# Optimization experiments

Hardware: AMD Instinct MI355X
Metric: run time of the kernel (lower is better)

The kernel has to match this reference:

```python
import jax, jax.numpy as jnp
import numpy as np

H, DK, DV, DEMB = 16, 64, 64, 1024
D_MODEL = H * DV


def setup_inputs() -> dict:
    key = jax.random.key(0)
    ks = jax.random.split(key, 9)
    scale = 0.02
    x = jax.random.normal(ks[0], (4, 2048, DEMB), dtype=jnp.float32)
    wq = jax.random.normal(ks[1], (DEMB, H * DK), dtype=jnp.float32) * scale
    bq = jnp.zeros((H * DK,), dtype=jnp.float32)
    wk = jax.random.normal(ks[2], (DEMB, H * DK), dtype=jnp.float32) * scale
    bk = jnp.zeros((H * DK,), dtype=jnp.float32)
    wv = jax.random.normal(ks[3], (DEMB, H * DV), dtype=jnp.float32) * scale
    bv = jnp.zeros((H * DV,), dtype=jnp.float32)
    wo = jax.random.normal(ks[4], (D_MODEL, D_MODEL), dtype=jnp.float32) * scale
    bo = jnp.zeros((D_MODEL,), dtype=jnp.float32)
    return {"x": x, "wq": wq, "bq": bq, "wk": wk, "bk": bk,
            "wv": wv, "bv": bv, "wo": wo, "bo": bo, "mask": 0}


def _split_heads(t, h):
    # (b, s, h*d) -> (b, h, s, d)
    b, s, _ = t.shape
    return t.reshape(b, s, h, -1).transpose(0, 2, 1, 3)


def reference(x, wq, bq, wk, bk, wv, bv, wo, bo, mask):
    b, s, _ = x.shape
    qs = _split_heads(x @ wq + bq, H)  # (b, h, s, dk)
    ks = _split_heads(x @ wk + bk, H)
    vs = _split_heads(x @ wv + bv, H)  # (b, h, s, dv)
    # FAITHFUL quirk: original scales by 1/sqrt(len(ks[0])) == 1/sqrt(n_heads),
    # not 1/sqrt(d_k).
    scores = jnp.einsum('bhqd,bhkd->bhqk', qs, ks) / jnp.sqrt(jnp.float32(H))
    # FAITHFUL quirk: masked_fill(mask == 0, ...) with scalar bool mask is a
    # no-op (True == 0 is False), so no masking is ever applied.
    attn = jax.nn.softmax(scores, axis=-1)
    out = jnp.einsum('bhqk,bhkd->bhqd', attn, vs)  # (b, h, s, dv)
    out = out.transpose(0, 2, 1, 3).reshape(b, s, D_MODEL)
    return out @ wo + bo
```

## Files before the change

### kernel.cpp

```cpp
#include <hip/hip_runtime.h>
#include <stdint.h>

typedef __attribute__((ext_vector_type(8))) short short8;
typedef __attribute__((ext_vector_type(4))) short short4v;
typedef __attribute__((ext_vector_type(4))) float floatx4;
typedef __attribute__((ext_vector_type(8))) _Float16 half8;
typedef __attribute__((ext_vector_type(2))) __fp16 pk2;

#define SEQ 2048
#define NTOK 8192
#define QSCALE 0.360673760222241f

__device__ __forceinline__ float b2f(unsigned short u){
  union { unsigned int i; float f; } v; v.i = ((unsigned int)u) << 16; return v.f;
}
__device__ __forceinline__ unsigned short f2b(float f){
  union { float f; unsigned int i; } v; v.f = f;
  unsigned int r = v.i + 0x7fffu + ((v.i >> 16) & 1u);
  return (unsigned short)(r >> 16);
}
__device__ __forceinline__ void async16(const unsigned short* g, unsigned short* l){
  __builtin_amdgcn_global_load_lds(
      (const __attribute__((address_space(1))) unsigned int*)g,
      (__attribute__((address_space(3))) unsigned int*)l, 16, 0, 0);
}

__global__ __launch_bounds__(256) void prep_kernel(
    const float* __restrict__ x,
    const float* __restrict__ wq, const float* __restrict__ wk,
    const float* __restrict__ wv, const float* __restrict__ wo,
    const float* __restrict__ bq, const float* __restrict__ bk,
    const float* __restrict__ bv,
    unsigned short* __restrict__ xb,
    unsigned short* __restrict__ wqkvT, unsigned short* __restrict__ woT,
    float* __restrict__ bqkv)
{
  __shared__ unsigned short lT[64][72];
  const int bid = blockIdx.x;
  const int tid = threadIdx.x;
  if (bid < 8192){
    int i = (bid*256 + tid)*4;
    float4 v = *(const float4*)(x + i);
    short4v o;
    o[0] = (short)f2b(v.x); o[1] = (short)f2b(v.y);
    o[2] = (short)f2b(v.z); o[3] = (short)f2b(v.w);
    *(short4v*)(xb + i) = o;
  } else if (bid < 9216){
    int idx = bid - 8192;
    int sel = idx >> 8, rest = idx & 255;
    const float* src = (sel==0)?wq:(sel==1)?wk:(sel==2)?wv:wo;
    unsigned short* dst = (sel<3) ? (wqkvT + (size_t)sel*1024*1024) : woT;
    int n0 = (rest & 15) * 64, k0 = (rest >> 4) * 64;
#pragma unroll
    for (int i=0;i<4;i++){
      int ch = tid + i*256;
      int r = ch>>4, c = (ch&15)*4;
      float4 v = *(const float4*)(src + (size_t)(k0+r)*1024 + n0 + c);
      lT[r][c+0] = f2b(v.x); lT[r][c+1] = f2b(v.y);
      lT[r][c+2] = f2b(v.z); lT[r][c+3] = f2b(v.w);
    }
    __syncthreads();
#pragma unroll
    for (int i=0;i<2;i++){
      int ch = tid + i*256;
      int rn = ch>>3, c = (ch&7)*8;
      short8 v;
#pragma unroll
      for (int j=0;j<8;j++) v[j] = (short)lT[c+j][rn];
      *(short8*)(dst + (size_t)(n0+rn)*1024 + k0 + c) = v;
    }
  } else {
    int i = (bid - 9216)*256 + tid;
    if (i < 3072){
      int sel = i >> 10, j = i & 1023;
      bqkv[i] = (sel==0)?bq[j]:(sel==1)?bk[j]:bv[j];
    }
  }
}

template<int MODE>
__global__ __launch_bounds__(256) void gemm_bt_kernel(
    const unsigned short* __restrict__ A,
    const unsigned short* __restrict__ Bt,
    const float* __restrict__ bias,
    void* __restrict__ Cv,
    unsigned short* __restrict__ Vt,
    int M, int N, int K)
{
  __shared__ unsigned short lA[128*64];
  __shared__ unsigned short lB[128*64];
  const int tid  = threadIdx.x;
  const int lane = tid & 63;
  const int wave = tid >> 6;
  const int quad = lane >> 4;
  const int l15  = lane & 15;
  const int wR = (wave >> 1) * 64;
  const int wC = (wave & 1) * 64;
  const int rowB = blockIdx.y * 128;
  const int colB = blockIdx.x * 128;

  const int srow = wave*32 + (lane>>3);
  const int sc8  = (lane&7) ^ (lane>>3);
  const unsigned short* gA = A  + (size_t)(rowB + srow)*K + sc8*8;
  const unsigned short* gB = Bt + (size_t)(colB + srow)*K + sc8*8;
  unsigned short* lAw = lA + wave*32*64 + lane*8;
  unsigned short* lBw = lB + wave*32*64 + lane*8;

  floatx4 acc[4][4];
#pragma unroll
  for (int t=0;t<4;t++)
#pragma unroll
    for (int u=0;u<4;u++) acc[t][u] = (floatx4){0.f,0.f,0.f,0.f};

  for (int kt = 0; kt < K; kt += 64){
    __syncthreads();
#pragma unroll
    for (int i=0;i<4;i++){
      async16(gA + (size_t)i*8*K + kt, lAw + i*512);
      async16(gB + (size_t)i*8*K + kt, lBw + i*512);
    }
    __syncthreads();
#pragma unroll
    for (int ks=0; ks<2; ks++){
      const int cph = ((ks*4 + quad) ^ (l15 & 7)) * 8;
      short8 af[4], bf[4];
#pragma unroll
      for (int t=0;t<4;t++) af[t] = *(const short8*)&lA[(wR + t*16 + l15)*64 + cph];
#pragma unroll
      for (int u=0;u<4;u++) bf[u] = *(const short8*)&lB[(wC + u*16 + l15)*64 + cph];
#pragma unroll
      for (int t=0;t<4;t++)
#pragma unroll
        for (int u=0;u<4;u++)
          acc[t][u] = __builtin_amdgcn_mfma_f32_16x16x32_bf16(af[t], bf[u], acc[t][u], 0, 0, 0);
    }
  }
  if (MODE == 3 && colB >= 2048){
#pragma unroll
    for (int u=0;u<4;u++){
      int col = colB + wC + u*16 + l15;
      float bval = bias[col];
      int vcol = col - 2048;
      int hh = vcol >> 6, dv = vcol & 63;
#pragma unroll
      for (int t=0;t<4;t++){
        int row0 = rowB + wR + t*16 + quad*4;
        int bb = row0 >> 11, s = row0 & 2047;
        union { pk2 p[2]; short4v s4; } cv;
        cv.p[0] = __builtin_amdgcn_cvt_pkrtz(acc[t][u][0]+bval, acc[t][u][1]+bval);
        cv.p[1] = __builtin_amdgcn_cvt_pkrtz(acc[t][u][2]+bval, acc[t][u][3]+bval);
        *(short4v*)(Vt + ((size_t)(bb*16+hh)*64 + dv)*2048 + s) = cv.s4;
      }
    }
  } else {
#pragma unroll
    for (int u=0;u<4;u++){
      int col = colB + wC + u*16 + l15;
      float bval = bias[col];
      float scale = (MODE == 3 && col < 1024) ? QSCALE : 1.0f;
#pragma unroll
      for (int t=0;t<4;t++){
        int row0 = rowB + wR + t*16 + quad*4;
#pragma unroll
        for (int r=0;r<4;r++){
          float val = (acc[t][u][r] + bval) * scale;
          if (MODE == 1) ((float*)Cv)[(size_t)(row0 + r)*N + col] = val;
          else ((unsigned short*)Cv)[(size_t)(row0 + r)*N + col] = f2b(val);
        }
      }
    }
  }
}

__global__ __launch_bounds__(256) void flash_attn_kernel(
    const unsigned short* __restrict__ qkv,
    const unsigned short* __restrict__ vt,
    unsigned short* __restrict__ attn_out)
{
  __shared__ __align__(16) unsigned short sK [2][64][64];
  __shared__ __align__(16) unsigned short sVt[2][64][64];
  const int bh = blockIdx.x;
  const int b = bh >> 4, h = bh & 15;
  const int qt = blockIdx.y;
  const int tid = threadIdx.x;
  const int wave = tid >> 6;
  const int lane = tid & 63;
  const int quad = lane >> 4, l15 = lane & 15;
  const int tok0 = b*SEQ + qt*128;

  short8 qf[2][2];
#pragma unroll
  for (int t=0;t<2;t++)
#pragma unroll
    for (int ks=0;ks<2;ks++)
      qf[t][ks] = *(const short8*)(qkv + (size_t)(tok0 + wave*32 + t*16 + l15)*3072
                                   + h*64 + ks*32 + quad*8);

  floatx4 oacc[2][4];
  float psum[2] = {0.f, 0.f};
#pragma unroll
  for (int t=0;t<2;t++)
#pragma unroll
    for (int v=0;v<4;v++) oacc[t][v] = (floatx4){0.f,0.f,0.f,0.f};

  int R[4], C[4], HF[4], SR[4], SWK[4], SWV[4];
#pragma unroll
  for (int i=0;i<4;i++){
    int chh = tid + (i&1)*256;
    R[i] = chh >> 3; C[i] = (chh & 7)*8; HF[i] = i >> 1;
    SR[i] = (R[i]&32) | ((R[i]&4)<<2) | ((R[i]>>1)&12) | (R[i]&3);
    SWK[i] = (((chh & 7) ^ (SR[i] & 7)) * 8);
    SWV[i] = (((chh & 7) ^ (R[i]  & 7)) * 8);
  }
  short8 rk[4], rv[4];
#pragma unroll
  for (int i=0;i<4;i++){
    rk[i] = *(const short8*)(qkv + (size_t)(b*SEQ + HF[i]*64 + R[i])*3072 + 1024 + h*64 + C[i]);
    rv[i] = *(const short8*)(vt  + (size_t)(bh*64 + R[i])*2048 + HF[i]*64 + C[i]);
  }

  for (int it = 0; it < SEQ/128; it++){
    __syncthreads();
#pragma unroll
    for (int i=0;i<4;i++){
      *(short8*)&sK [HF[i]][SR[i]][SWK[i]] = rk[i];
      *(short8*)&sVt[HF[i]][R[i] ][SWV[i]] = rv[i];
    }
    __syncthreads();
    if (it + 1 < SEQ/128){
      int nx = (it + 1) * 128;
#pragma unroll
      for (int i=0;i<4;i++){
        rk[i] = *(const short8*)(qkv + (size_t)(b*SEQ + nx + HF[i]*64 + R[i])*3072 + 1024 + h*64 + C[i]);
        rv[i] = *(const short8*)(vt  + (size_t)(bh*64 + R[i])*2048 + nx + HF[i]*64 + C[i]);
      }
    }

#pragma unroll
    for (int hf=0; hf<2; hf++){
      floatx4 sacc[4][2];
#pragma unroll
      for (int u=0;u<4;u++)
#pragma unroll
        for (int t=0;t<2;t++) sacc[u][t] = (floatx4){0.f,0.f,0.f,0.f};
#pragma unroll
      for (int ks=0;ks<2;ks++){
        short8 kf[4];
#pragma unroll
        for (int u=0;u<4;u++)
          kf[u] = *(const short8*)&sK[hf][u*16 + l15][((ks*4 + quad) ^ (l15 & 7)) * 8];
#pragma unroll
        for (int u=0;u<4;u++)
#pragma unroll
          for (int t=0;t<2;t++)
            sacc[u][t] = __builtin_amdgcn_mfma_f32_16x16x32_bf16(kf[u], qf[t][ks], sacc[u][t], 0,0,0);
      }

      unsigned pw[4][2][2];
#pragma unroll
      for (int t=0;t<2;t++){
#pragma unroll
        for (int u=0;u<4;u++){
          float p0 = __builtin_amdgcn_exp2f(sacc[u][t][0]);
          float p1 = __builtin_amdgcn_exp2f(sacc[u][t][1]);
          float p2 = __builtin_amdgcn_exp2f(sacc[u][t][2]);
          float p3 = __builtin_amdgcn_exp2f(sacc[u][t][3]);
          psum[t] += (p0+p1)+(p2+p3);
          union { pk2 p; unsigned u32; } c0, c1;
          c0.p = __builtin_amdgcn_cvt_pkrtz(p0,p1);
          c1.p = __builtin_amdgcn_cvt_pkrtz(p2,p3);
          pw[u][t][0] = c0.u32; pw[u][t][1] = c1.u32;
        }
      }
      half8 pf[2][2];
#pragma unroll
      for (int t=0;t<2;t++)
#pragma unroll
        for (int B=0;B<2;B++){
          union { unsigned u32[4]; half8 h; } a;
          a.u32[0] = pw[2*B  ][t][0]; a.u32[1] = pw[2*B  ][t][1];
          a.u32[2] = pw[2*B+1][t][0]; a.u32[3] = pw[2*B+1][t][1];
          pf[t][B] = a.h;
        }

#pragma unroll
      for (int v=0;v<4;v++){
#pragma unroll
        for (int B=0;B<2;B++){
          union { short8 s; half8 h; } vb;
          vb.s = *(const short8*)&sVt[hf][v*16 + l15][((B*4 + quad) ^ (l15 & 7)) * 8];
#pragma unroll
          for (int t=0;t<2;t++)
            oacc[t][v] = __builtin_amdgcn_mfma_f32_16x16x32_f16(pf[t][B], vb.h, oacc[t][v], 0,0,0);
        }
      }
    }
  }

#pragma unroll
  for (int t=0;t<2;t++){
    float s = psum[t];
    s += __shfl_xor(s, 16);
    s += __shfl_xor(s, 32);
    psum[t] = s;
  }
#pragma unroll
  for (int t=0;t<2;t++){
#pragma unroll
    for (int r=0;r<4;r++){
      float inv = 1.0f / __shfl(psum[t], quad*4 + r);
      int tok = tok0 + wave*32 + t*16 + quad*4 + r;
#pragma unroll
      for (int v=0;v<4;v++)
        attn_out[(size_t)tok*1024 + h*64 + v*16 + l15] = f2b(oacc[t][v][r] * inv);
    }
  }
}

extern "C" void kernel_launch(void* const* d_in, const int* in_sizes, int n_in,
                              void* d_out, int out_size, void* d_ws, size_t ws_size,
                              hipStream_t stream)
{
  const float* x  = (const float*)d_in[0];
  const float* wq = (const float*)d_in[1];
  const float* bq = (const float*)d_in[2];
  const float* wk = (const float*)d_in[3];
  const float* bk = (const float*)d_in[4];
  const float* wv = (const float*)d_in[5];
  const float* bv = (const float*)d_in[6];
  const float* wo = (const float*)d_in[7];
  const float* bo = (const float*)d_in[8];
  float* out = (float*)d_out;

  char* ws = (char*)d_ws;
  unsigned short* wqkvT  = (unsigned short*)(ws);
  unsigned short* woT    = (unsigned short*)(ws + 6291456);
  float*          bqkv   = (float*)(ws + 8388608);
  unsigned short* xb     = (unsigned short*)(ws + 8400896);
  unsigned short* qkvbuf = (unsigned short*)(ws + 25178112);
  unsigned short* vtbuf  = (unsigned short*)(ws + 75509760);
  unsigned short* aobuf  = (unsigned short*)(ws + 92286976);

  prep_kernel<<<dim3(9228), 256, 0, stream>>>(x, wq, wk, wv, wo, bq, bk, bv,
                                              xb, wqkvT, woT, bqkv);
  gemm_bt_kernel<3><<<dim3(24, 64), 256, 0, stream>>>(xb, wqkvT, bqkv, qkvbuf, vtbuf,
                                                      8192, 3072, 1024);
  flash_attn_kernel<<<dim3(64, 16), 256, 0, stream>>>(qkvbuf, vtbuf, aobuf);
  gemm_bt_kernel<1><<<dim3(8, 64), 256, 0, stream>>>(aobuf, woT, bo, out, nullptr,
                                                     8192, 1024, 1024);
}
```

Baseline: 295.5 us.

## Use 512-thread attention blocks with 256 queries and double-buffered K/V tiles

Doubles the flash-attention block to 8 waves covering 256 query rows, so each K/V tile staged in LDS is shared by twice as many queries and the grid halves. The LDS tiles become a ping-pong pair indexed by iteration parity, which drops one __syncthreads per iteration. Staging addresses are precomputed as base pointers and offsets. In exchange, LDS use per block grows and only 512 blocks are launched, which may lower occupancy and CU balance.

```diff
diff --git a/kernel.cpp b/kernel.cpp
--- a/kernel.cpp
+++ b/kernel.cpp
@@ -172,13 +172,13 @@
   }
 }
 
-__global__ __launch_bounds__(256) void flash_attn_kernel(
+__global__ __launch_bounds__(512) void flash_attn_kernel(
     const unsigned short* __restrict__ qkv,
     const unsigned short* __restrict__ vt,
     unsigned short* __restrict__ attn_out)
 {
-  __shared__ __align__(16) unsigned short sK [2][64][64];
-  __shared__ __align__(16) unsigned short sVt[2][64][64];
+  __shared__ __align__(16) unsigned short sK [2][128][64];
+  __shared__ __align__(16) unsigned short sVt[2][64][128];
   const int bh = blockIdx.x;
   const int b = bh >> 4, h = bh & 15;
   const int qt = blockIdx.y;
@@ -186,7 +186,7 @@
   const int wave = tid >> 6;
   const int lane = tid & 63;
   const int quad = lane >> 4, l15 = lane & 15;
-  const int tok0 = b*SEQ + qt*128;
+  const int tok0 = b*SEQ + qt*256;
 
   short8 qf[2][2];
 #pragma unroll
@@ -203,36 +203,42 @@
 #pragma unroll
     for (int v=0;v<4;v++) oacc[t][v] = (floatx4){0.f,0.f,0.f,0.f};
 
-  int R[4], C[4], HF[4], SR[4], SWK[4], SWV[4];
-#pragma unroll
-  for (int i=0;i<4;i++){
-    int chh = tid + (i&1)*256;
-    R[i] = chh >> 3; C[i] = (chh & 7)*8; HF[i] = i >> 1;
-    SR[i] = (R[i]&32) | ((R[i]&4)<<2) | ((R[i]>>1)&12) | (R[i]&3);
-    SWK[i] = (((chh & 7) ^ (SR[i] & 7)) * 8);
-    SWV[i] = (((chh & 7) ^ (R[i]  & 7)) * 8);
-  }
-  short8 rk[4], rv[4];
-#pragma unroll
-  for (int i=0;i<4;i++){
-    rk[i] = *(const short8*)(qkv + (size_t)(b*SEQ + HF[i]*64 + R[i])*3072 + 1024 + h*64 + C[i]);
-    rv[i] = *(const short8*)(vt  + (size_t)(bh*64 + R[i])*2048 + HF[i]*64 + C[i]);
+  const unsigned short* kbase[2]; const unsigned short* vbase[2];
+  int KD[2], VD[2];
+#pragma unroll
+  for (int i=0;i<2;i++){
+    int c = tid + i*512;
+    int kr = c >> 3, kc = c & 7;
+    int sr = (kr & 96) | ((kr & 4) << 2) | ((kr >> 1) & 12) | (kr & 3);
+    kbase[i] = qkv + (size_t)(b*SEQ + kr)*3072 + 1024 + h*64 + kc*8;
+    KD[i] = sr*64 + ((kc ^ (sr & 7)) * 8);
+    int dv = c >> 4, vc = c & 15;
+    int hfb = vc >> 3, c3 = vc & 7;
+    vbase[i] = vt + (size_t)(bh*64 + dv)*2048 + vc*8;
+    VD[i] = dv*128 + (hfb*8 + (c3 ^ (dv & 7))) * 8;
+  }
+  short8 rk[2], rv[2];
+#pragma unroll
+  for (int i=0;i<2;i++){
+    rk[i] = *(const short8*)(kbase[i]);
+    rv[i] = *(const short8*)(vbase[i]);
   }
 
   for (int it = 0; it < SEQ/128; it++){
-    __syncthreads();
-#pragma unroll
-    for (int i=0;i<4;i++){
-      *(short8*)&sK [HF[i]][SR[i]][SWK[i]] = rk[i];
-      *(short8*)&sVt[HF[i]][R[i] ][SWV[i]] = rv[i];
+    unsigned short* sKb = &sK [it & 1][0][0];
+    unsigned short* sVb = &sVt[it & 1][0][0];
+#pragma unroll
+    for (int i=0;i<2;i++){
+      *(short8*)(sKb + KD[i]) = rk[i];
+      *(short8*)(sVb + VD[i]) = rv[i];
     }
     __syncthreads();
     if (it + 1 < SEQ/128){
       int nx = (it + 1) * 128;
 #pragma unroll
-      for (int i=0;i<4;i++){
-        rk[i] = *(const short8*)(qkv + (size_t)(b*SEQ + nx + HF[i]*64 + R[i])*3072 + 1024 + h*64 + C[i]);
-        rv[i] = *(const short8*)(vt  + (size_t)(bh*64 + R[i])*2048 + nx + HF[i]*64 + C[i]);
+      for (int i=0;i<2;i++){
+        rk[i] = *(const short8*)(kbase[i] + (size_t)nx*3072);
+        rv[i] = *(const short8*)(vbase[i] + nx);
       }
     }
 
@@ -248,7 +254,8 @@
         short8 kf[4];
 #pragma unroll
         for (int u=0;u<4;u++)
-          kf[u] = *(const short8*)&sK[hf][u*16 + l15][((ks*4 + quad) ^ (l15 & 7)) * 8];
+          kf[u] = *(const short8*)(sKb + (hf*64 + u*16 + l15)*64
+                                   + ((ks*4 + quad) ^ (l15 & 7)) * 8);
 #pragma unroll
         for (int u=0;u<4;u++)
 #pragma unroll
@@ -288,7 +295,8 @@
 #pragma unroll
         for (int B=0;B<2;B++){
           union { short8 s; half8 h; } vb;
-          vb.s = *(const short8*)&sVt[hf][v*16 + l15][((B*4 + quad) ^ (l15 & 7)) * 8];
+          vb.s = *(const short8*)(sVb + (v*16 + l15)*128
+                                  + (hf*8 + ((B*4 + quad) ^ (l15 & 7))) * 8);
 #pragma unroll
           for (int t=0;t<2;t++)
             oacc[t][v] = __builtin_amdgcn_mfma_f32_16x16x32_f16(pf[t][B], vb.h, oacc[t][v], 0,0,0);
@@ -345,7 +353,7 @@
                                               xb, wqkvT, woT, bqkv);
   gemm_bt_kernel<3><<<dim3(24, 64), 256, 0, stream>>>(xb, wqkvT, bqkv, qkvbuf, vtbuf,
                                                       8192, 3072, 1024);
-  flash_attn_kernel<<<dim3(64, 16), 256, 0, stream>>>(qkvbuf, vtbuf, aobuf);
+  flash_attn_kernel<<<dim3(64, 8), 512, 0, stream>>>(qkvbuf, vtbuf, aobuf);
   gemm_bt_kernel<1><<<dim3(8, 64), 256, 0, stream>>>(aobuf, woT, bo, out, nullptr,
                                                      8192, 1024, 1024);
 }
```

Result: faster. 273.5 us (-7.4%).
